# Kernel tuning notes

Measured on AMD Instinct MI355X. Metric: run time of the kernel, lower is better.

## Reference

```python
import jax, jax.numpy as jnp
import numpy as np

B, T, IN_DIM, H = 128, 512, 128, 512


def _lstm_layer(x, W_ih, W_hh, b_ih, b_hh):
    """Single-layer batch-first LSTM (PyTorch gate order i,f,g,o).
    x: [B, T, D]. Returns (outputs [B, T, H], h_T [B, H], c_T [B, H])."""
    Bsz = x.shape[0]
    Hdim = W_hh.shape[1]
    # Precompute the input contribution for all timesteps: [T, B, 4H]
    xg = jnp.einsum('btd,gd->tbg', x, W_ih) + (b_ih + b_hh)

    def step(carry, xg_t):
        h, c = carry
        gates = xg_t + h @ W_hh.T  # [B, 4H]
        i, f, g, o = jnp.split(gates, 4, axis=-1)
        i = jax.nn.sigmoid(i)
        f = jax.nn.sigmoid(f)
        g = jnp.tanh(g)
        o = jax.nn.sigmoid(o)
        c = f * c + i * g
        h = o * jnp.tanh(c)
        return (h, c), h

    h0 = jnp.zeros((Bsz, Hdim), dtype=x.dtype)
    c0 = jnp.zeros((Bsz, Hdim), dtype=x.dtype)
    (hT, cT), outs = jax.lax.scan(step, (h0, c0), xg)
    return jnp.transpose(outs, (1, 0, 2)), hT, cT


def setup_inputs() -> dict:
    key = jax.random.key(0)
    ks = jax.random.split(key, 9)
    s1 = 1.0 / np.sqrt(H)
    inp = {
        'x': jax.random.normal(ks[0], (B, T, IN_DIM), dtype=jnp.float32),
        'W_ih1': jax.random.uniform(ks[1], (4 * H, IN_DIM), jnp.float32, -s1, s1),
        'W_hh1': jax.random.uniform(ks[2], (4 * H, H), jnp.float32, -s1, s1),
        'b_ih1': jax.random.uniform(ks[3], (4 * H,), jnp.float32, -s1, s1),
        'b_hh1': jax.random.uniform(ks[4], (4 * H,), jnp.float32, -s1, s1),
        'W_ih2': jax.random.uniform(ks[5], (4 * H, H), jnp.float32, -s1, s1),
        'W_hh2': jax.random.uniform(ks[6], (4 * H, H), jnp.float32, -s1, s1),
        'b_ih2': jax.random.uniform(ks[7], (4 * H,), jnp.float32, -s1, s1),
        'b_hh2': jax.random.uniform(ks[8], (4 * H,), jnp.float32, -s1, s1),
    }
    return inp


def reference(x, W_ih1, W_hh1, b_ih1, b_hh1, W_ih2, W_hh2, b_ih2, b_hh2):
    out1, _, _ = _lstm_layer(x, W_ih1, W_hh1, b_ih1, b_hh1)
    _, hT, cT = _lstm_layer(out1, W_ih2, W_hh2, b_ih2, b_hh2)
    # Match torch nn.LSTM final-state shape: [num_layers*dirs=1, B, H]
    return hT[None, :, :], cT[None, :, :]
```

## Files before the change

kernel.cpp:

```cpp
#include <hip/hip_runtime.h>
#include <stdint.h>
#include <stddef.h>


typedef __attribute__((ext_vector_type(8))) short short8;
typedef __attribute__((ext_vector_type(4))) float f32x4;
typedef unsigned long long u64;

#define DEV static __device__ __forceinline__
#define SCOPE_AGENT __HIP_MEMORY_SCOPE_AGENT

constexpr int TSEQ = 512;
constexpr int DIN  = 128;
constexpr int HDIM = 512;
constexpr int NCL  = 8;
constexpr int BB   = 16;
constexpr int NJ   = 32;
constexpr int COLS = 16;

DEV unsigned short f2bf(float f) {
  unsigned u = __float_as_uint(f);
  u += 0x7fffu + ((u >> 16) & 1u);
  return (unsigned short)(u >> 16);
}
DEV short8 pack8(float4 a, float4 b) {
  short8 r;
  r[0] = (short)f2bf(a.x); r[1] = (short)f2bf(a.y);
  r[2] = (short)f2bf(a.z); r[3] = (short)f2bf(a.w);
  r[4] = (short)f2bf(b.x); r[5] = (short)f2bf(b.y);
  r[6] = (short)f2bf(b.z); r[7] = (short)f2bf(b.w);
  return r;
}
DEV short8 mk8(u64 lo, u64 hi) {
  union { u64 q[2]; short8 v; } u;
  u.q[0] = lo; u.q[1] = hi; return u.v;
}
DEV f32x4 mfma16(short8 a, short8 b, f32x4 c) {
  return __builtin_amdgcn_mfma_f32_16x16x32_bf16(a, b, c, 0, 0, 0);
}
DEV float sigf(float v) { return 1.f / (1.f + __expf(-v)); }
DEV float tanh_(float v) {
  v = fminf(20.f, fmaxf(-20.f, v));
  float e = __expf(2.f * v);
  return (e - 1.f) / (e + 1.f);
}

__global__ void zero_ws(unsigned* p, int n) {
  int i = blockIdx.x * 256 + threadIdx.x;
  if (i < n)
    __hip_atomic_store(p + i, 0u, __ATOMIC_RELAXED, SCOPE_AGENT);
}

#define SWZ(row, idx) ((idx) ^ (((row) & 15) << 3))

__global__ __launch_bounds__(256, 1) void lstm_persist(
    const float* __restrict__ x,
    const float* __restrict__ Wih1, const float* __restrict__ Whh1,
    const float* __restrict__ bih1, const float* __restrict__ bhh1,
    const float* __restrict__ Wih2, const float* __restrict__ Whh2,
    const float* __restrict__ bih2, const float* __restrict__ bhh2,
    float* __restrict__ out,
    unsigned short* __restrict__ buf1,
    unsigned short* __restrict__ buf2,
    unsigned* __restrict__ flags)
{
  __shared__ short xs [16 * DIN];
  __shared__ short h1s[16 * HDIM];
  __shared__ short h2s[16 * HDIM];
  __shared__ float red1[4 * 16 * 68];
  __shared__ float red2[4 * 16 * 68];
  __shared__ float bias1s[64], bias2s[64];
  __shared__ float occpad[3072];

  const int tid  = threadIdx.x;
  const int lane = tid & 63;
  const int lm   = lane & 15;
  const int lq   = lane >> 4;
  const int kq   = tid >> 6;

  const int bid     = blockIdx.x;
  const int cluster = bid & 7;
  const int j       = bid >> 3;
  const int cb      = cluster * BB;
  unsigned* flagA = flags + cluster * 64;
  unsigned* flagB = flags + cluster * 64 + NJ;

  asm volatile("" :: "v"(&occpad[tid & 1023]));

  short8 wf1[4][5];
  short8 wf2[4][8];
  #pragma unroll
  for (int g = 0; g < 4; ++g) {
    const int gr = g * HDIM + j * COLS + lm;
    #pragma unroll
    for (int sl = 0; sl < 5; ++sl) {
      const int k0 = (kq * 5 + sl) * 32 + 8 * lq;
      const float* src = (k0 < DIN) ? (Wih1 + (size_t)gr * DIN + k0)
                                    : (Whh1 + (size_t)gr * HDIM + (k0 - DIN));
      wf1[g][sl] = pack8(*(const float4*)src, *(const float4*)(src + 4));
    }
    #pragma unroll
    for (int sl = 0; sl < 8; ++sl) {
      const int k0 = (kq * 8 + sl) * 32 + 8 * lq;
      const float* src = (k0 < HDIM) ? (Wih2 + (size_t)gr * HDIM + k0)
                                     : (Whh2 + (size_t)gr * HDIM + (k0 - HDIM));
      wf2[g][sl] = pack8(*(const float4*)src, *(const float4*)(src + 4));
    }
  }
  if (tid < 64) {
    const int g = tid >> 4, nn = tid & 15;
    const int gr = g * HDIM + j * COLS + nn;
    bias1s[tid] = bih1[gr] + bhh1[gr];
    bias2s[tid] = bih2[gr] + bhh2[gr];
  }

  const int pm = tid >> 4, pnn = tid & 15;
  float c1 = 0.f, c2 = 0.f;

  const int lr   = lane >> 4;
  const int skc  = kq * 16 + (lane & 15);
  const int prod = skc >> 1;

  for (int it = 0; it <= TSEQ; ++it) {
    const bool l1 = (it < TSEQ);
    const bool l2 = (it >= 1);

    float4 xa, xb;
    if (l1) {
      const int row = tid >> 4, kc16 = tid & 15;
      const float* xp = x + ((size_t)(cb + row) * TSEQ + it) * DIN + kc16 * 8;
      xa = *(const float4*)xp; xb = *(const float4*)(xp + 4);
    }

    const unsigned short* h1r =
        buf1 + (size_t)(((it + 1) & 1) * NCL + cluster) * BB * HDIM;
    const unsigned short* h2r =
        buf2 + (size_t)((it & 1) * NCL + cluster) * BB * HDIM;
    if (it > 0) {
      const unsigned tgA = (unsigned)(it < TSEQ ? it : TSEQ);
      const unsigned tgB = (unsigned)(it - 1);
      const unsigned* fA = flagA + prod;
      const unsigned* fB = flagB + prod;
      while (true) {
        unsigned a = __hip_atomic_load(fA, __ATOMIC_RELAXED, SCOPE_AGENT);
        unsigned b = __hip_atomic_load(fB, __ATOMIC_RELAXED, SCOPE_AGENT);
        if (a >= tgA && b >= tgB) break;
        __builtin_amdgcn_s_sleep(1);
      }
    }
    {
      u64 t1[8], t2[8];
      #pragma unroll
      for (int ci = 0; ci < 4; ++ci) {
        const int row = ci * 4 + lr;
        const u64* s = (const u64*)(h1r + (size_t)row * HDIM + skc * 8);
        t1[2 * ci]     = __hip_atomic_load(s,     __ATOMIC_RELAXED, SCOPE_AGENT);
        t1[2 * ci + 1] = __hip_atomic_load(s + 1, __ATOMIC_RELAXED, SCOPE_AGENT);
      }
      #pragma unroll
      for (int ci = 0; ci < 4; ++ci) {
        const int row = ci * 4 + lr;
        const u64* s = (const u64*)(h2r + (size_t)row * HDIM + skc * 8);
        t2[2 * ci]     = __hip_atomic_load(s,     __ATOMIC_RELAXED, SCOPE_AGENT);
        t2[2 * ci + 1] = __hip_atomic_load(s + 1, __ATOMIC_RELAXED, SCOPE_AGENT);
      }
      #pragma unroll
      for (int ci = 0; ci < 4; ++ci) {
        const int row = ci * 4 + lr;
        *(short8*)(&h1s[SWZ(row, row * HDIM + skc * 8)]) =
            mk8(t1[2 * ci], t1[2 * ci + 1]);
      }
      #pragma unroll
      for (int ci = 0; ci < 4; ++ci) {
        const int row = ci * 4 + lr;
        *(short8*)(&h2s[SWZ(row, row * HDIM + skc * 8)]) =
            mk8(t2[2 * ci], t2[2 * ci + 1]);
      }
    }
    if (l1) {
      const int row = tid >> 4, kc16 = tid & 15;
      *(short8*)(&xs[SWZ(row, row * DIN + kc16 * 8)]) = pack8(xa, xb);
    }
    __syncthreads();

    f32x4 z = {0.f, 0.f, 0.f, 0.f};
    f32x4 acc1[4] = {z, z, z, z};
    f32x4 acc2[4] = {z, z, z, z};
    if (l1) {
      #pragma unroll
      for (int sl = 0; sl < 5; ++sl) {
        const int s = kq * 5 + sl;
        short8 a;
        if (s < 4)
          a = *(const short8*)(&xs[SWZ(lm, lm * DIN + s * 32 + 8 * lq)]);
        else
          a = *(const short8*)(&h1s[SWZ(lm, lm * HDIM + (s - 4) * 32 + 8 * lq)]);
        #pragma unroll
        for (int g = 0; g < 4; ++g) acc1[g] = mfma16(a, wf1[g][sl], acc1[g]);
      }
    }
    if (l2) {
      #pragma unroll
      for (int sl = 0; sl < 8; ++sl) {
        const int s2 = kq * 8 + sl;
        short8 a;
        if (s2 < 16)
          a = *(const short8*)(&h1s[SWZ(lm, lm * HDIM + s2 * 32 + 8 * lq)]);
        else
          a = *(const short8*)(&h2s[SWZ(lm, lm * HDIM + (s2 - 16) * 32 + 8 * lq)]);
        #pragma unroll
        for (int g = 0; g < 4; ++g) acc2[g] = mfma16(a, wf2[g][sl], acc2[g]);
      }
    }
    if (l1) {
      #pragma unroll
      for (int g = 0; g < 4; ++g)
        #pragma unroll
        for (int r = 0; r < 4; ++r)
          red1[(kq * 16 + lq * 4 + r) * 68 + g * 16 + lm] = acc1[g][r];
    }
    if (l2) {
      #pragma unroll
      for (int g = 0; g < 4; ++g)
        #pragma unroll
        for (int r = 0; r < 4; ++r)
          red2[(kq * 16 + lq * 4 + r) * 68 + g * 16 + lm] = acc2[g][r];
    }
    __syncthreads();

    if (l1) {
      float p[4];
      #pragma unroll
      for (int g = 0; g < 4; ++g) {
        float v = bias1s[g * 16 + pnn];
        #pragma unroll
        for (int q = 0; q < 4; ++q) v += red1[(q * 16 + pm) * 68 + g * 16 + pnn];
        p[g] = v;
      }
      const float i_ = sigf(p[0]), f_ = sigf(p[1]);
      const float g_ = tanh_(p[2]), o_ = sigf(p[3]);
      c1 = f_ * c1 + i_ * g_;
      const float h1v = o_ * tanh_(c1);
      unsigned short* wp = buf1 + (size_t)((it & 1) * NCL + cluster) * BB * HDIM;
      __hip_atomic_store(&wp[pm * HDIM + j * COLS + pnn], f2bf(h1v),
                         __ATOMIC_RELAXED, SCOPE_AGENT);
    }
    __syncthreads();
    if (tid == 0 && l1)
      __hip_atomic_store(flagA + j, (unsigned)(it + 1),
                         __ATOMIC_RELAXED, SCOPE_AGENT);

    if (l2) {
      float p[4];
      #pragma unroll
      for (int g = 0; g < 4; ++g) {
        float v = bias2s[g * 16 + pnn];
        #pragma unroll
        for (int q = 0; q < 4; ++q) v += red2[(q * 16 + pm) * 68 + g * 16 + pnn];
        p[g] = v;
      }
      const float i_ = sigf(p[0]), f_ = sigf(p[1]);
      const float g_ = tanh_(p[2]), o_ = sigf(p[3]);
      c2 = f_ * c2 + i_ * g_;
      const float h2v = o_ * tanh_(c2);
      if (l1) {
        unsigned short* wp =
            buf2 + (size_t)(((it + 1) & 1) * NCL + cluster) * BB * HDIM;
        __hip_atomic_store(&wp[pm * HDIM + j * COLS + pnn], f2bf(h2v),
                           __ATOMIC_RELAXED, SCOPE_AGENT);
      } else {
        const int b = cb + pm;
        out[(size_t)b * HDIM + j * COLS + pnn] = h2v;
        out[(size_t)128 * HDIM + (size_t)b * HDIM + j * COLS + pnn] = c2;
      }
    }
    __syncthreads();
    if (tid == 0 && l1 && l2)
      __hip_atomic_store(flagB + j, (unsigned)it,
                         __ATOMIC_RELAXED, SCOPE_AGENT);
  }
}

extern "C" void kernel_launch(void* const* d_in, const int* in_sizes, int n_in,
                              void* d_out, int out_size, void* d_ws, size_t ws_size,
                              hipStream_t stream) {
  const float* x    = (const float*)d_in[0];
  const float* Wih1 = (const float*)d_in[1];
  const float* Whh1 = (const float*)d_in[2];
  const float* bih1 = (const float*)d_in[3];
  const float* bhh1 = (const float*)d_in[4];
  const float* Wih2 = (const float*)d_in[5];
  const float* Whh2 = (const float*)d_in[6];
  const float* bih2 = (const float*)d_in[7];
  const float* bhh2 = (const float*)d_in[8];
  float* out = (float*)d_out;

  const size_t bufElems = (size_t)2 * NCL * BB * HDIM;
  unsigned short* buf1 = (unsigned short*)d_ws;
  unsigned short* buf2 = buf1 + bufElems;
  unsigned* flags = (unsigned*)(buf2 + bufElems);

  const int nzero = (int)((bufElems * 2 * 2 + NCL * 64 * 4) / 4);
  zero_ws<<<(nzero + 255) / 256, 256, 0, stream>>>((unsigned*)d_ws, nzero);
  lstm_persist<<<256, 256, 0, stream>>>(x, Wih1, Whh1, bih1, bhh1,
                                        Wih2, Whh2, bih2, bhh2,
                                        out, buf1, buf2, flags);
}
```

Measured before the change: 1.892 ms.

## Replace per-block flags with per-wave flags to drop end-of-step barriers

Each wave now publishes its own completion flag for the rows it wrote, after a vmcnt wait, instead of the whole block doing __syncthreads and then tid 0 setting one flag. The output rows per wave are remapped so each wave owns four batch rows, and consumers poll the per-wave flag matching the rows they read. This removes two block-wide barriers per timestep from the serial recurrence critical path. In exchange there are four times as many flag stores and a larger flag array. The next iteration may still race on the red buffers, since one of the barriers that protected their reuse is gone.

```diff
diff --git a/kernel.cpp b/kernel.cpp
--- a/kernel.cpp
+++ b/kernel.cpp
@@ -82,8 +82,8 @@
   const int cluster = bid & 7;
   const int j       = bid >> 3;
   const int cb      = cluster * BB;
-  unsigned* flagA = flags + cluster * 64;
-  unsigned* flagB = flags + cluster * 64 + NJ;
+  unsigned* flagA4 = flags + cluster * 256;
+  unsigned* flagB4 = flags + cluster * 256 + 128;
 
   asm volatile("" :: "v"(&occpad[tid & 1023]));
 
@@ -114,7 +114,8 @@
     bias2s[tid] = bih2[gr] + bhh2[gr];
   }
 
-  const int pm = tid >> 4, pnn = tid & 15;
+  const int prow = ((tid >> 4) & 3) * 4 + kq;
+  const int pnn  = tid & 15;
   float c1 = 0.f, c2 = 0.f;
 
   const int lr   = lane >> 4;
@@ -139,8 +140,8 @@
     if (it > 0) {
       const unsigned tgA = (unsigned)(it < TSEQ ? it : TSEQ);
       const unsigned tgB = (unsigned)(it - 1);
-      const unsigned* fA = flagA + prod;
-      const unsigned* fB = flagB + prod;
+      const unsigned* fA = flagA4 + prod * 4 + lr;
+      const unsigned* fB = flagB4 + prod * 4 + lr;
       while (true) {
         unsigned a = __hip_atomic_load(fA, __ATOMIC_RELAXED, SCOPE_AGENT);
         unsigned b = __hip_atomic_load(fB, __ATOMIC_RELAXED, SCOPE_AGENT);
@@ -234,7 +235,8 @@
       for (int g = 0; g < 4; ++g) {
         float v = bias1s[g * 16 + pnn];
         #pragma unroll
-        for (int q = 0; q < 4; ++q) v += red1[(q * 16 + pm) * 68 + g * 16 + pnn];
+        for (int q = 0; q < 4; ++q)
+          v += red1[(q * 16 + prow) * 68 + g * 16 + pnn];
         p[g] = v;
       }
       const float i_ = sigf(p[0]), f_ = sigf(p[1]);
@@ -242,21 +244,21 @@
       c1 = f_ * c1 + i_ * g_;
       const float h1v = o_ * tanh_(c1);
       unsigned short* wp = buf1 + (size_t)((it & 1) * NCL + cluster) * BB * HDIM;
-      __hip_atomic_store(&wp[pm * HDIM + j * COLS + pnn], f2bf(h1v),
+      __hip_atomic_store(&wp[prow * HDIM + j * COLS + pnn], f2bf(h1v),
                          __ATOMIC_RELAXED, SCOPE_AGENT);
-    }
-    __syncthreads();
-    if (tid == 0 && l1)
-      __hip_atomic_store(flagA + j, (unsigned)(it + 1),
-                         __ATOMIC_RELAXED, SCOPE_AGENT);
-
+      asm volatile("s_waitcnt vmcnt(0)" ::: "memory");
+      if (lane == 0)
+        __hip_atomic_store(flagA4 + j * 4 + kq, (unsigned)(it + 1),
+                           __ATOMIC_RELAXED, SCOPE_AGENT);
+    }
     if (l2) {
       float p[4];
       #pragma unroll
       for (int g = 0; g < 4; ++g) {
         float v = bias2s[g * 16 + pnn];
         #pragma unroll
-        for (int q = 0; q < 4; ++q) v += red2[(q * 16 + pm) * 68 + g * 16 + pnn];
+        for (int q = 0; q < 4; ++q)
+          v += red2[(q * 16 + prow) * 68 + g * 16 + pnn];
         p[g] = v;
       }
       const float i_ = sigf(p[0]), f_ = sigf(p[1]);
@@ -266,18 +268,18 @@
       if (l1) {
         unsigned short* wp =
             buf2 + (size_t)(((it + 1) & 1) * NCL + cluster) * BB * HDIM;
-        __hip_atomic_store(&wp[pm * HDIM + j * COLS + pnn], f2bf(h2v),
+        __hip_atomic_store(&wp[prow * HDIM + j * COLS + pnn], f2bf(h2v),
                            __ATOMIC_RELAXED, SCOPE_AGENT);
+        asm volatile("s_waitcnt vmcnt(0)" ::: "memory");
+        if (lane == 0)
+          __hip_atomic_store(flagB4 + j * 4 + kq, (unsigned)it,
+                             __ATOMIC_RELAXED, SCOPE_AGENT);
       } else {
-        const int b = cb + pm;
+        const int b = cb + prow;
         out[(size_t)b * HDIM + j * COLS + pnn] = h2v;
         out[(size_t)128 * HDIM + (size_t)b * HDIM + j * COLS + pnn] = c2;
       }
     }
-    __syncthreads();
-    if (tid == 0 && l1 && l2)
-      __hip_atomic_store(flagB + j, (unsigned)it,
-                         __ATOMIC_RELAXED, SCOPE_AGENT);
   }
 }
 
@@ -300,7 +302,7 @@
   unsigned short* buf2 = buf1 + bufElems;
   unsigned* flags = (unsigned*)(buf2 + bufElems);
 
-  const int nzero = (int)((bufElems * 2 * 2 + NCL * 64 * 4) / 4);
+  const int nzero = (int)((bufElems * 2 * 2 + NCL * 256 * 4) / 4);
   zero_ws<<<(nzero + 255) / 256, 256, 0, stream>>>((unsigned*)d_ws, nzero);
   lstm_persist<<<256, 256, 0, stream>>>(x, Wih1, Whh1, bih1, bhh1,
                                         Wih2, Whh2, bih2, bhh2,
```

Result: slower. 3.228 ms (+70.6%).
